# Kernel tuning notes

Hardware: AMD Instinct MI355X
Metric: run time of the kernel (lower is better)

The kernel has to match this reference:

```python
import jax, jax.numpy as jnp
import numpy as np

B, H, S, Q = 32768, 896, 448, 256  # batch, hidden, split=hidden//2, quantisation


def setup_inputs() -> dict:
    key = jax.random.key(0)
    ks = jax.random.split(key, 16)
    sc = 0.02
    return {
        'prev_y': jax.random.uniform(ks[0], (B, 2), jnp.float32) * 2.0 - 1.0,
        'prev_hidden': jax.random.normal(ks[1], (B, H), jnp.float32),
        'current_coarse': jax.random.uniform(ks[2], (B, 1), jnp.float32) * 2.0 - 1.0,
        'W_R': jax.random.normal(ks[3], (H, 3 * H), jnp.float32) * sc,
        'W_Ic': jax.random.normal(ks[4], (2, 3 * S), jnp.float32) * sc,
        'W_If': jax.random.normal(ks[5], (3, 3 * S), jnp.float32) * sc,
        'W_O1': jax.random.normal(ks[6], (S, S), jnp.float32) * sc,
        'b_O1': jnp.zeros((S,), jnp.float32),
        'W_O2': jax.random.normal(ks[7], (S, Q), jnp.float32) * sc,
        'b_O2': jnp.zeros((Q,), jnp.float32),
        'W_O3': jax.random.normal(ks[8], (S, S), jnp.float32) * sc,
        'b_O3': jnp.zeros((S,), jnp.float32),
        'W_O4': jax.random.normal(ks[9], (S, Q), jnp.float32) * sc,
        'b_O4': jnp.zeros((Q,), jnp.float32),
        'bias_u': jnp.zeros((H,), jnp.float32),
        'bias_r': jnp.zeros((H,), jnp.float32),
        'bias_e': jnp.zeros((H,), jnp.float32),
    }


def reference(prev_y, prev_hidden, current_coarse, W_R, W_Ic, W_If,
              W_O1, b_O1, W_O2, b_O2, W_O3, b_O3, W_O4, b_O4,
              bias_u, bias_r, bias_e):
    # recurrent projection of previous hidden state: [B, 3H]
    R_u, R_r, R_e = jnp.split(prev_hidden @ W_R, 3, axis=1)
    # coarse-half input projection from (prev_coarse, prev_fine): [B, 3S]
    I_cu, I_cr, I_ce = jnp.split(prev_y @ W_Ic, 3, axis=1)
    # fine-half input projection from (prev_coarse, prev_fine, current_coarse): [B, 3S]
    fine_in = jnp.concatenate([prev_y, current_coarse], axis=1)
    I_fu, I_fr, I_fe = jnp.split(fine_in @ W_If, 3, axis=1)
    I_u = jnp.concatenate([I_cu, I_fu], axis=1)
    I_r = jnp.concatenate([I_cr, I_fr], axis=1)
    I_e = jnp.concatenate([I_ce, I_fe], axis=1)
    u = jax.nn.sigmoid(R_u + I_u + bias_u)
    r = jax.nn.sigmoid(R_r + I_r + bias_r)
    e = jnp.tanh(r * R_e + I_e + bias_e)
    hidden = u * prev_hidden + (1.0 - u) * e
    h_c, h_f = jnp.split(hidden, 2, axis=1)
    out_coarse = jax.nn.relu(h_c @ W_O1 + b_O1) @ W_O2 + b_O2
    out_fine = jax.nn.relu(h_f @ W_O3 + b_O3) @ W_O4 + b_O4
    return out_coarse, out_fine, hidden
```

## Files before the change

kernel.cpp:

```cpp
#include <hip/hip_runtime.h>


typedef unsigned short u16;
typedef unsigned int u32;
typedef __attribute__((ext_vector_type(8))) short bf16x8;
typedef __attribute__((ext_vector_type(4))) float f32x4;

#define GAS __attribute__((address_space(1)))
#define LAS __attribute__((address_space(3)))

__device__ __forceinline__ u16 f2b(float f) {
  union { float f; u32 i; } v; v.f = f;
  return (u16)((v.i + 0x7fffu + ((v.i >> 16) & 1u)) >> 16);
}

__device__ __forceinline__ void gl_lds(const u16* g, u16* l) {
  __builtin_amdgcn_global_load_lds((const GAS void*)g, (LAS void*)l, 16, 0, 0);
}

__global__ void cvt_f32_bf16(const float* __restrict__ in, u16* __restrict__ outp) {
  const size_t i = ((size_t)blockIdx.x * 256 + threadIdx.x) * 4;
  const float4 v = *(const float4*)&in[i];
  ushort4 o;
  o.x = f2b(v.x); o.y = f2b(v.y); o.z = f2b(v.z); o.w = f2b(v.w);
  *(ushort4*)&outp[i] = o;
}

__device__ __forceinline__ void transpose_body(const float* __restrict__ in,
                                               u16* __restrict__ outp,
                                               int R, int C, int c0, int r0) {
  __shared__ u16 t[32][33];
  const int x = threadIdx.x, y = threadIdx.y;
  #pragma unroll
  for (int i = 0; i < 32; i += 8)
    t[y + i][x] = f2b(in[(size_t)(r0 + y + i) * C + (c0 + x)]);
  __syncthreads();
  #pragma unroll
  for (int i = 0; i < 32; i += 8)
    outp[(size_t)(c0 + y + i) * R + (r0 + x)] = t[x][y + i];
}

__global__ void transpose_f32_bf16(const float* __restrict__ in, u16* __restrict__ outp,
                                   int R, int C) {
  transpose_body(in, outp, R, C, blockIdx.x * 32, blockIdx.y * 32);
}

__global__ void transpose_wo(const float* __restrict__ w1, const float* __restrict__ w2,
                             const float* __restrict__ w3, const float* __restrict__ w4,
                             u16* __restrict__ o1, u16* __restrict__ o2,
                             u16* __restrict__ o3, u16* __restrict__ o4) {
  const int z = blockIdx.z;
  const float* in = (z == 0) ? w1 : (z == 1) ? w2 : (z == 2) ? w3 : w4;
  u16* outp = (z == 0) ? o1 : (z == 1) ? o2 : (z == 2) ? o3 : o4;
  const int C = (z & 1) ? 256 : 448;
  const int c0 = blockIdx.x * 32;
  if (c0 >= C) return;
  transpose_body(in, outp, 448, C, c0, blockIdx.y * 32);
}

__device__ __forceinline__ void gemm_tile_k(const u16* __restrict__ A, int lda,
                                            const u16* __restrict__ BT, int ldb,
                                            int K, u16* Al, u16* Bl,
                                            int wave, int lane, f32x4 (&acc)[4][4]) {
  const int wm = wave & 1, wn = wave >> 1;
  const int q = lane >> 4, l16 = lane & 15;
  const int sr = lane >> 2;
  const int sc = (lane & 3) * 8;
  for (int k0 = 0; k0 < K; k0 += 32) {
    #pragma unroll
    for (int i = 0; i < 2; ++i) {
      const int rr = wave * 32 + i * 16;
      gl_lds(A + (size_t)(rr + sr) * lda + (k0 + sc), &Al[rr * 32]);
      gl_lds(BT + (size_t)(rr + sr) * ldb + (k0 + sc), &Bl[rr * 32]);
    }
    __syncthreads();
    bf16x8 af[4], bfr[4];
    #pragma unroll
    for (int t = 0; t < 4; ++t) {
      af[t]  = *(const bf16x8*)&Al[(wm * 64 + t * 16 + l16) * 32 + q * 8];
      bfr[t] = *(const bf16x8*)&Bl[(wn * 64 + t * 16 + l16) * 32 + q * 8];
    }
    #pragma unroll
    for (int mt = 0; mt < 4; ++mt)
      #pragma unroll
      for (int nt = 0; nt < 4; ++nt)
        acc[mt][nt] = __builtin_amdgcn_mfma_f32_16x16x32_bf16(af[mt], bfr[nt],
                                                              acc[mt][nt], 0, 0, 0);
    __syncthreads();
  }
}

__device__ __forceinline__ void zero_acc(f32x4 (&acc)[4][4]) {
  const f32x4 z = {0.f, 0.f, 0.f, 0.f};
  #pragma unroll
  for (int mt = 0; mt < 4; ++mt)
    #pragma unroll
    for (int nt = 0; nt < 4; ++nt)
      acc[mt][nt] = z;
}

__global__ __launch_bounds__(1024, 4)
void gate_kernel(const u16* __restrict__ phb, const u16* __restrict__ wrt,
                 const float* __restrict__ phf,
                 const float* __restrict__ y2, const float* __restrict__ cc,
                 const float* __restrict__ wic, const float* __restrict__ wif,
                 const float* __restrict__ bu, const float* __restrict__ br,
                 const float* __restrict__ be,
                 float* __restrict__ houtf, u16* __restrict__ hb) {
  __shared__ u16 Sl[3][16384];
  __shared__ float rowy[3 * 128];
  const int tid = threadIdx.x;
  const int lane = tid & 63, wave = tid >> 6;
  const int f = blockIdx.x;
  const int xcd = f & 7, l = f >> 3;
  const int m0 = (xcd * 32 + (l & 31)) * 128;
  const int j0 = (l >> 5) * 128;
  if (tid < 128) {
    const int r = m0 + tid;
    rowy[tid]       = y2[2 * r];
    rowy[128 + tid] = y2[2 * r + 1];
    rowy[256 + tid] = cc[r];
    asm volatile("s_waitcnt lgkmcnt(0)" ::: "memory");
  }
  const int wm = wave & 3, wn = wave >> 2;
  const int q = lane >> 4, l16 = lane & 15;
  const int sr = lane >> 2, sc = (lane & 3) * 8;

  const int u0 = 2 * wave, u1 = u0 + 1;
  const u16* g0; const u16* g1; int lo0, lo1;
  if (u0 < 8) { g0 = phb + (size_t)(m0 + u0 * 16 + sr) * 896 + sc; lo0 = u0 * 512; }
  else { const int nn = u0 - 8, jj = nn / 3, s = nn % 3;
         g0 = wrt + (size_t)(s * 896 + j0 + jj * 16 + sr) * 896 + sc;
         lo0 = 4096 + nn * 512; }
  if (u1 < 8) { g1 = phb + (size_t)(m0 + u1 * 16 + sr) * 896 + sc; lo1 = u1 * 512; }
  else { const int nn = u1 - 8, jj = nn / 3, s = nn % 3;
         g1 = wrt + (size_t)(s * 896 + j0 + jj * 16 + sr) * 896 + sc;
         lo1 = 4096 + nn * 512; }

  f32x4 acc[2][3][2];
  {
    const f32x4 z = {0.f, 0.f, 0.f, 0.f};
    #pragma unroll
    for (int a = 0; a < 2; ++a)
      #pragma unroll
      for (int s = 0; s < 3; ++s)
        #pragma unroll
        for (int m = 0; m < 2; ++m)
          acc[a][s][m] = z;
  }

  auto stage = [&](int t_) {
    const int b_ = t_ % 3;
    const int k_ = t_ * 32;
    gl_lds(g0 + k_, &Sl[b_][lo0]);
    gl_lds(g1 + k_, &Sl[b_][lo1]);
  };

  stage(0);
  stage(1);
  for (int t = 0; t < 28; ++t) {
    if (t < 27) asm volatile("s_waitcnt vmcnt(2)" ::: "memory");
    else        asm volatile("s_waitcnt vmcnt(0)" ::: "memory");
    __builtin_amdgcn_s_barrier();
    __builtin_amdgcn_sched_barrier(0);
    const u16* Sb = Sl[t % 3];
    bf16x8 af[2];
    #pragma unroll
    for (int mt = 0; mt < 2; ++mt)
      af[mt] = *(const bf16x8*)&Sb[(wm * 32 + mt * 16 + l16) * 32 + q * 8];
    #pragma unroll
    for (int jj2 = 0; jj2 < 2; ++jj2)
      #pragma unroll
      for (int s = 0; s < 3; ++s) {
        const int nn = (2 * wn + jj2) * 3 + s;
        const bf16x8 bf_ = *(const bf16x8*)&Sb[4096 + nn * 512 + l16 * 32 + q * 8];
        #pragma unroll
        for (int mt = 0; mt < 2; ++mt)
          acc[jj2][s][mt] = __builtin_amdgcn_mfma_f32_16x16x32_bf16(
              af[mt], bf_, acc[jj2][s][mt], 0, 0, 0);
      }
    if (t + 2 < 28) stage(t + 2);
  }

  #pragma unroll
  for (int jj2 = 0; jj2 < 2; ++jj2) {
    const int j = j0 + (2 * wn + jj2) * 16 + l16;
    float wu0, wu1, wu2, wr0, wr1, wr2, we0, we1, we2;
    if (j < 448) {
      wu0 = wic[j];       wu1 = wic[1344 + j];       wu2 = 0.f;
      wr0 = wic[448 + j]; wr1 = wic[1792 + j];       wr2 = 0.f;
      we0 = wic[896 + j]; we1 = wic[2240 + j];       we2 = 0.f;
    } else {
      const int jf = j - 448;
      wu0 = wif[jf];       wu1 = wif[1344 + jf]; wu2 = wif[2688 + jf];
      wr0 = wif[448 + jf]; wr1 = wif[1792 + jf]; wr2 = wif[3136 + jf];
      we0 = wif[896 + jf]; we1 = wif[2240 + jf]; we2 = wif[3584 + jf];
    }
    const float bju = bu[j], bjr = br[j], bje = be[j];
    #pragma unroll
    for (int mt = 0; mt < 2; ++mt) {
      const int rl = wm * 32 + mt * 16 + q * 4;
      #pragma unroll
      for (int i = 0; i < 4; ++i) {
        const float y0 = rowy[rl + i], y1 = rowy[128 + rl + i], yc = rowy[256 + rl + i];
        const float gu = acc[jj2][0][mt][i] + y0 * wu0 + y1 * wu1 + yc * wu2 + bju;
        const float gr = acc[jj2][1][mt][i] + y0 * wr0 + y1 * wr1 + yc * wr2 + bjr;
        const float uu = 1.f / (1.f + __expf(-gu));
        const float rg = 1.f / (1.f + __expf(-gr));
        const float ev = tanhf(rg * acc[jj2][2][mt][i] +
                               y0 * we0 + y1 * we1 + yc * we2 + bje);
        const size_t grow = (size_t)(m0 + rl + i);
        const float phv = phf[grow * 896 + j];
        const float h = uu * phv + (1.f - uu) * ev;
        houtf[grow * 896 + j] = h;
        hb[grow * 896 + j] = f2b(h);
      }
    }
  }
}

__global__ __launch_bounds__(256, 2)
void stage1_kernel(const u16* __restrict__ hb, const u16* __restrict__ w1t,
                   const u16* __restrict__ w3t, const float* __restrict__ b1,
                   const float* __restrict__ b3, u16* __restrict__ tc,
                   u16* __restrict__ tf) {
  __shared__ u16 Al[128 * 32];
  __shared__ u16 Bl[128 * 32];
  const int tid = threadIdx.x, lane = tid & 63, wave = tid >> 6;
  const int f = blockIdx.x;
  const int xcd = f & 7, l = f >> 3;
  const int mz = xcd * 64 + (l >> 2);
  const int z = mz >> 8;
  const int m0 = (mz & 255) * 128, n0 = (l & 3) * 128;
  const u16* A = hb + (size_t)m0 * 896 + z * 448;
  const u16* BT = (z ? w3t : w1t) + (size_t)n0 * 448;
  const float* bias = z ? b3 : b1;
  u16* T = z ? tf : tc;
  const int wm = wave & 1, wn = wave >> 1, q = lane >> 4, l16 = lane & 15;
  f32x4 acc[4][4];
  zero_acc(acc);
  gemm_tile_k(A, 896, BT, 448, 448, Al, Bl, wave, lane, acc);
  #pragma unroll
  for (int nt = 0; nt < 4; ++nt) {
    const int j = n0 + wn * 64 + nt * 16 + l16;
    if (j < 448) {
      const float bv = bias[j];
      #pragma unroll
      for (int mt = 0; mt < 4; ++mt)
        #pragma unroll
        for (int i = 0; i < 4; ++i) {
          const size_t row = (size_t)(m0 + wm * 64 + mt * 16 + q * 4 + i);
          T[row * 448 + j] = f2b(fmaxf(acc[mt][nt][i] + bv, 0.f));
        }
    }
  }
}

__global__ __launch_bounds__(256, 2)
void stage2_kernel(const u16* __restrict__ tc, const u16* __restrict__ tf,
                   const u16* __restrict__ w2t, const u16* __restrict__ w4t,
                   const float* __restrict__ b2_, const float* __restrict__ b4,
                   float* __restrict__ out) {
  __shared__ u16 Al[128 * 32];
  __shared__ u16 Bl[128 * 32];
  const int tid = threadIdx.x, lane = tid & 63, wave = tid >> 6;
  const int f = blockIdx.x;
  const int xcd = f & 7, l = f >> 3;
  const int mz = xcd * 64 + (l >> 1);
  const int z = mz >> 8;
  const int m0 = (mz & 255) * 128, n0 = (l & 1) * 128;
  const u16* A = (z ? tf : tc) + (size_t)m0 * 448;
  const u16* BT = (z ? w4t : w2t) + (size_t)n0 * 448;
  const float* bias = z ? b4 : b2_;
  float* O = out + (size_t)z * 32768 * 256;
  const int wm = wave & 1, wn = wave >> 1, q = lane >> 4, l16 = lane & 15;
  f32x4 acc[4][4];
  zero_acc(acc);
  gemm_tile_k(A, 448, BT, 448, 448, Al, Bl, wave, lane, acc);
  #pragma unroll
  for (int nt = 0; nt < 4; ++nt) {
    const int j = n0 + wn * 64 + nt * 16 + l16;
    const float bv = bias[j];
    #pragma unroll
    for (int mt = 0; mt < 4; ++mt)
      #pragma unroll
      for (int i = 0; i < 4; ++i) {
        const size_t row = (size_t)(m0 + wm * 64 + mt * 16 + q * 4 + i);
        O[row * 256 + j] = acc[mt][nt][i] + bv;
      }
  }
}

extern "C" void kernel_launch(void* const* d_in, const int* in_sizes, int n_in,
                              void* d_out, int out_size, void* d_ws, size_t ws_size,
                              hipStream_t stream) {
  const float* y2   = (const float*)d_in[0];
  const float* ph   = (const float*)d_in[1];
  const float* cc   = (const float*)d_in[2];
  const float* W_R  = (const float*)d_in[3];
  const float* W_Ic = (const float*)d_in[4];
  const float* W_If = (const float*)d_in[5];
  const float* W_O1 = (const float*)d_in[6];
  const float* b_O1 = (const float*)d_in[7];
  const float* W_O2 = (const float*)d_in[8];
  const float* b_O2 = (const float*)d_in[9];
  const float* W_O3 = (const float*)d_in[10];
  const float* b_O3 = (const float*)d_in[11];
  const float* W_O4 = (const float*)d_in[12];
  const float* b_O4 = (const float*)d_in[13];
  const float* bu   = (const float*)d_in[14];
  const float* br   = (const float*)d_in[15];
  const float* be   = (const float*)d_in[16];
  float* out = (float*)d_out;
  u16* ws  = (u16*)d_ws;

  u16* WRT = ws;
  u16* W1T = WRT + (size_t)2688 * 896;
  u16* W2T = W1T + 448 * 448;
  u16* W3T = W2T + 256 * 448;
  u16* W4T = W3T + 448 * 448;
  u16* phb = W4T + 256 * 448;
  u16* hb  = phb + (size_t)32768 * 896;
  u16* Tc  = phb;
  u16* Tf  = phb + (size_t)32768 * 448;
  float* hidf = out + (size_t)2 * 32768 * 256;

  dim3 tb(32, 8);
  cvt_f32_bf16<<<28672, 256, 0, stream>>>(ph, phb);
  transpose_f32_bf16<<<dim3(2688 / 32, 896 / 32), tb, 0, stream>>>(W_R, WRT, 896, 2688);
  transpose_wo<<<dim3(14, 14, 4), tb, 0, stream>>>(W_O1, W_O2, W_O3, W_O4,
                                                   W1T, W2T, W3T, W4T);

  gate_kernel<<<1792, 1024, 0, stream>>>(phb, WRT, ph, y2, cc, W_Ic, W_If,
                                         bu, br, be, hidf, hb);
  stage1_kernel<<<2048, 256, 0, stream>>>(hb, W1T, W3T, b_O1, b_O3, Tc, Tf);
  stage2_kernel<<<1024, 256, 0, stream>>>(Tc, Tf, W2T, W4T, b_O2, b_O4, out);
}
```

Before: 628.9 us.

## Shrink gate tile to 64 rows, load A directly to registers, swizzle B in LDS

The gate GEMM tile goes from 128x128 (1024 threads) to 64x128 (512 threads) with twice as many blocks. The A operand (prev_hidden bf16) is now read straight from global memory into registers and double-buffered, while only the W_R tiles are staged through LDS with an XOR swizzle meant to reduce bank conflicts. The goal is to cut LDS traffic and footprint, raise occupancy and reduce bank conflicts. The cost is that each block reuses A across fewer columns, and direct global A loads may be less coalesced.

```diff
diff --git a/kernel.cpp b/kernel.cpp
--- a/kernel.cpp
+++ b/kernel.cpp
@@ -99,7 +99,7 @@
       acc[mt][nt] = z;
 }
 
-__global__ __launch_bounds__(1024, 4)
+__global__ __launch_bounds__(512, 4)
 void gate_kernel(const u16* __restrict__ phb, const u16* __restrict__ wrt,
                  const float* __restrict__ phf,
                  const float* __restrict__ y2, const float* __restrict__ cc,
@@ -107,35 +107,37 @@
                  const float* __restrict__ bu, const float* __restrict__ br,
                  const float* __restrict__ be,
                  float* __restrict__ houtf, u16* __restrict__ hb) {
-  __shared__ u16 Sl[3][16384];
-  __shared__ float rowy[3 * 128];
+  __shared__ u16 Bl[3][12288];
+  __shared__ float rowy[3 * 64];
   const int tid = threadIdx.x;
   const int lane = tid & 63, wave = tid >> 6;
   const int f = blockIdx.x;
   const int xcd = f & 7, l = f >> 3;
-  const int m0 = (xcd * 32 + (l & 31)) * 128;
-  const int j0 = (l >> 5) * 128;
-  if (tid < 128) {
+  const int m0 = (xcd * 64 + l / 7) * 64;
+  const int j0 = (l % 7) * 128;
+  if (tid < 64) {
     const int r = m0 + tid;
-    rowy[tid]       = y2[2 * r];
-    rowy[128 + tid] = y2[2 * r + 1];
-    rowy[256 + tid] = cc[r];
+    rowy[tid]      = y2[2 * r];
+    rowy[64 + tid] = y2[2 * r + 1];
+    rowy[128 + tid] = cc[r];
     asm volatile("s_waitcnt lgkmcnt(0)" ::: "memory");
   }
-  const int wm = wave & 3, wn = wave >> 2;
+  const int wm = wave & 1, wn = wave >> 1;
   const int q = lane >> 4, l16 = lane & 15;
-  const int sr = lane >> 2, sc = (lane & 3) * 8;
-
-  const int u0 = 2 * wave, u1 = u0 + 1;
-  const u16* g0; const u16* g1; int lo0, lo1;
-  if (u0 < 8) { g0 = phb + (size_t)(m0 + u0 * 16 + sr) * 896 + sc; lo0 = u0 * 512; }
-  else { const int nn = u0 - 8, jj = nn / 3, s = nn % 3;
-         g0 = wrt + (size_t)(s * 896 + j0 + jj * 16 + sr) * 896 + sc;
-         lo0 = 4096 + nn * 512; }
-  if (u1 < 8) { g1 = phb + (size_t)(m0 + u1 * 16 + sr) * 896 + sc; lo1 = u1 * 512; }
-  else { const int nn = u1 - 8, jj = nn / 3, s = nn % 3;
-         g1 = wrt + (size_t)(s * 896 + j0 + jj * 16 + sr) * 896 + sc;
-         lo1 = 4096 + nn * 512; }
+  const int qs = q ^ ((l16 >> 1) & 3);
+  const int sr = lane >> 2;
+  const int sc = ((lane & 3) ^ ((lane >> 3) & 3)) * 8;
+
+  const u16* ag = phb + (size_t)(m0 + wm * 32 + l16) * 896 + q * 8;
+
+  const u16* gs[3]; int lo[3];
+  #pragma unroll
+  for (int i = 0; i < 3; ++i) {
+    const int nn = 3 * wave + i;
+    const int s = nn % 3, jj = nn / 3;
+    gs[i] = wrt + (size_t)(s * 896 + j0 + jj * 16 + sr) * 896 + sc;
+    lo[i] = nn * 512;
+  }
 
   f32x4 acc[2][3][2];
   {
@@ -150,37 +152,47 @@
   }
 
   auto stage = [&](int t_) {
-    const int b_ = t_ % 3;
-    const int k_ = t_ * 32;
-    gl_lds(g0 + k_, &Sl[b_][lo0]);
-    gl_lds(g1 + k_, &Sl[b_][lo1]);
+    u16* base = &Bl[t_ % 3][0];
+    const int koff = t_ * 32;
+    #pragma unroll
+    for (int i = 0; i < 3; ++i) gl_lds(gs[i] + koff, base + lo[i]);
   };
 
-  stage(0);
-  stage(1);
-  for (int t = 0; t < 28; ++t) {
-    if (t < 27) asm volatile("s_waitcnt vmcnt(2)" ::: "memory");
-    else        asm volatile("s_waitcnt vmcnt(0)" ::: "memory");
-    __builtin_amdgcn_s_barrier();
-    __builtin_amdgcn_sched_barrier(0);
-    const u16* Sb = Sl[t % 3];
-    bf16x8 af[2];
-    #pragma unroll
-    for (int mt = 0; mt < 2; ++mt)
-      af[mt] = *(const bf16x8*)&Sb[(wm * 32 + mt * 16 + l16) * 32 + q * 8];
-    #pragma unroll
-    for (int jj2 = 0; jj2 < 2; ++jj2)
-      #pragma unroll
-      for (int s = 0; s < 3; ++s) {
-        const int nn = (2 * wn + jj2) * 3 + s;
-        const bf16x8 bf_ = *(const bf16x8*)&Sb[4096 + nn * 512 + l16 * 32 + q * 8];
-        #pragma unroll
-        for (int mt = 0; mt < 2; ++mt)
-          acc[jj2][s][mt] = __builtin_amdgcn_mfma_f32_16x16x32_bf16(
-              af[mt], bf_, acc[jj2][s][mt], 0, 0, 0);
-      }
-    if (t + 2 < 28) stage(t + 2);
-  }
+  stage(0); stage(1);
+  bf16x8 afA[2], afB[2];
+  afA[0] = *(const bf16x8*)(ag);
+  afA[1] = *(const bf16x8*)(ag + (size_t)16 * 896);
+
+  #define GATE_BODY(T, AFU, AFL)                                               \
+    {                                                                          \
+      const int t = (T);                                                       \
+      asm volatile("s_waitcnt vmcnt(3)" ::: "memory");                         \
+      __builtin_amdgcn_s_barrier();                                            \
+      __builtin_amdgcn_sched_barrier(0);                                       \
+      const int tn = (t + 1 < 28) ? t + 1 : 27;                                \
+      AFL[0] = *(const bf16x8*)(ag + tn * 32);                                 \
+      AFL[1] = *(const bf16x8*)(ag + (size_t)16 * 896 + tn * 32);              \
+      stage(t + 2 < 27 ? t + 2 : 27);                                          \
+      const u16* Sb = &Bl[t % 3][0];                                           \
+      _Pragma("unroll")                                                        \
+      for (int jj2 = 0; jj2 < 2; ++jj2)                                        \
+        _Pragma("unroll")                                                      \
+        for (int s = 0; s < 3; ++s) {                                          \
+          const int nn = (2 * wn + jj2) * 3 + s;                               \
+          const bf16x8 bf_ = *(const bf16x8*)&Sb[nn * 512 + l16 * 32 + qs * 8];\
+          _Pragma("unroll")                                                    \
+          for (int mt = 0; mt < 2; ++mt)                                       \
+            acc[jj2][s][mt] = __builtin_amdgcn_mfma_f32_16x16x32_bf16(         \
+                AFU[mt], bf_, acc[jj2][s][mt], 0, 0, 0);                       \
+        }                                                                      \
+    }
+
+  for (int tt = 0; tt < 14; ++tt) {
+    GATE_BODY(2 * tt,     afA, afB)
+    GATE_BODY(2 * tt + 1, afB, afA)
+  }
+  #undef GATE_BODY
+  asm volatile("s_waitcnt vmcnt(0)" ::: "memory");
 
   #pragma unroll
   for (int jj2 = 0; jj2 < 2; ++jj2) {
@@ -202,7 +214,7 @@
       const int rl = wm * 32 + mt * 16 + q * 4;
       #pragma unroll
       for (int i = 0; i < 4; ++i) {
-        const float y0 = rowy[rl + i], y1 = rowy[128 + rl + i], yc = rowy[256 + rl + i];
+        const float y0 = rowy[rl + i], y1 = rowy[64 + rl + i], yc = rowy[128 + rl + i];
         const float gu = acc[jj2][0][mt][i] + y0 * wu0 + y1 * wu1 + yc * wu2 + bju;
         const float gr = acc[jj2][1][mt][i] + y0 * wr0 + y1 * wr1 + yc * wr2 + bjr;
         const float uu = 1.f / (1.f + __expf(-gu));
@@ -331,8 +343,8 @@
   transpose_wo<<<dim3(14, 14, 4), tb, 0, stream>>>(W_O1, W_O2, W_O3, W_O4,
                                                    W1T, W2T, W3T, W4T);
 
-  gate_kernel<<<1792, 1024, 0, stream>>>(phb, WRT, ph, y2, cc, W_Ic, W_If,
-                                         bu, br, be, hidf, hb);
+  gate_kernel<<<3584, 512, 0, stream>>>(phb, WRT, ph, y2, cc, W_Ic, W_If,
+                                        bu, br, be, hidf, hb);
   stage1_kernel<<<2048, 256, 0, stream>>>(hb, W1T, W3T, b_O1, b_O3, Tc, Tf);
   stage2_kernel<<<1024, 256, 0, stream>>>(Tc, Tf, W2T, W4T, b_O2, b_O4, out);
 }
```

Result: slower. 738.3 us (+17.4%).
